# Kernel optimization log

Measured on AMD Instinct MI355X. Metric: run time of the kernel, lower is better.

Reference implementation:

```python
import jax, jax.numpy as jnp
import numpy as np

K = 1.0          # manifold curvature parameter (Lorentz hyperboloid <x,x>_L = -K)
NUM_HEADS = 16
LN_EPS = 1e-5
MID_EPS = 1e-8


def add_time(space):
    # lift a space-like vector onto the hyperboloid: x0 = sqrt(||s||^2 + K)
    t = jnp.sqrt(jnp.sum(space * space, axis=-1, keepdims=True) + K)
    return jnp.concatenate([t, space], axis=-1)


def hlinear(x, W, b):
    # Lorentz linear: dense map on full ambient vector -> space part, recompute time
    return add_time(jnp.einsum('...d,od->...o', x, W) + b)


def hyp_layernorm(x, g, b):
    s = x[..., 1:]
    mu = jnp.mean(s, axis=-1, keepdims=True)
    var = jnp.mean((s - mu) ** 2, axis=-1, keepdims=True)
    s = (s - mu) * jax.lax.rsqrt(var + LN_EPS) * g + b
    return add_time(s)


def hyp_relu(x):
    return add_time(jax.nn.relu(x[..., 1:]))


def lorentz_norm(v):
    # sqrt(|<v,v>_L|) with clamp for numerical safety
    inner = -v[..., 0] ** 2 + jnp.sum(v[..., 1:] ** 2, axis=-1)
    return jnp.sqrt(jnp.maximum(jnp.abs(inner), MID_EPS))


def midpoint_pair(z, x):
    # manifold.midpoint(stack([z, x], dim=-2)).squeeze(): mean then project back
    ave = 0.5 * (z + x)
    return jnp.sqrt(K) * ave / lorentz_norm(ave)[..., None]


def attention(x, Wq, bq, Wk, bk, Wv, bv, Wo, bo):
    B, S, D = x.shape
    dim = D - 1
    H = NUM_HEADS
    dh = dim // H

    def split_heads(t):
        # drop time, split space into heads, re-lift each head onto hyperboloid
        s = t[..., 1:].reshape(B, S, H, dh).transpose(0, 2, 1, 3)  # [B,H,S,dh]
        return add_time(s)                                          # [B,H,S,dh+1]

    qh = split_heads(hlinear(x, Wq, bq))
    kh = split_heads(hlinear(x, Wk, bk))
    vh = split_heads(hlinear(x, Wv, bv))

    # pairwise Lorentz inner product; scores = -d_L^2 / sqrt(dh)
    inner = (jnp.einsum('bhid,bhjd->bhij', qh[..., 1:], kh[..., 1:])
             - qh[..., 0][..., :, None] * kh[..., 0][..., None, :])
    scores = (2.0 / K + 2.0 * inner) / jnp.sqrt(jnp.asarray(dh, x.dtype))
    att = jax.nn.softmax(scores, axis=-1)

    # Lorentz midpoint aggregation of values (weights sum to 1)
    ave = jnp.einsum('bhij,bhjd->bhid', att, vh)
    out = jnp.sqrt(K) * ave / lorentz_norm(ave)[..., None]  # [B,H,S,dh+1]

    # concat head space parts, re-lift, output projection
    out_space = out[..., 1:].transpose(0, 2, 1, 3).reshape(B, S, dim)
    return hlinear(add_time(out_space), Wo, bo)


def reference(x, Wq, bq, Wk, bk, Wv, bv, Wo, bo, ln1_g, ln1_b, W1, c1, W2, c2, ln2_g, ln2_b):
    z = attention(x, Wq, bq, Wk, bk, Wv, bv, Wo, bo)
    x = midpoint_pair(z, x)
    x = hyp_layernorm(x, ln1_g, ln1_b)
    h = hyp_relu(hlinear(x, W1, c1))
    z = hlinear(h, W2, c2)
    x = midpoint_pair(z, x)
    x = hyp_layernorm(x, ln2_g, ln2_b)
    return x


def setup_inputs() -> dict:
    key = jax.random.key(0)
    ks = jax.random.split(key, 12)
    B, S, dim, mlp = 4, 1024, 1024, 4096
    D = dim + 1
    sc = 0.02
    x = add_time(jax.random.normal(ks[0], (B, S, dim), dtype=jnp.float32))
    return {
        'x': x,
        'Wq': sc * jax.random.normal(ks[1], (dim, D), dtype=jnp.float32),
        'bq': jnp.zeros((dim,), jnp.float32),
        'Wk': sc * jax.random.normal(ks[2], (dim, D), dtype=jnp.float32),
        'bk': jnp.zeros((dim,), jnp.float32),
        'Wv': sc * jax.random.normal(ks[3], (dim, D), dtype=jnp.float32),
        'bv': jnp.zeros((dim,), jnp.float32),
        'Wo': sc * jax.random.normal(ks[4], (dim, D), dtype=jnp.float32),
        'bo': jnp.zeros((dim,), jnp.float32),
        'ln1_g': jnp.ones((dim,), jnp.float32),
        'ln1_b': jnp.zeros((dim,), jnp.float32),
        'W1': sc * jax.random.normal(ks[5], (mlp, D), dtype=jnp.float32),
        'c1': jnp.zeros((mlp,), jnp.float32),
        'W2': sc * jax.random.normal(ks[6], (dim, mlp + 1), dtype=jnp.float32),
        'c2': jnp.zeros((dim,), jnp.float32),
        'ln2_g': jnp.ones((dim,), jnp.float32),
        'ln2_b': jnp.zeros((dim,), jnp.float32),
    }
```

## Files before the change

### kernel.cpp

```cpp
#include <hip/hip_runtime.h>

typedef unsigned short u16;
typedef unsigned int   u32;
typedef short bf16x8 __attribute__((ext_vector_type(8)));
typedef float f32x4  __attribute__((ext_vector_type(4)));

#define NTOK 4096
#define SEQ  1024

__device__ __forceinline__ u16 f2bf(float f){
  union { float f; u32 u; } x; x.f = f;
  u32 r = (x.u + 0x7FFFu + ((x.u >> 16) & 1u)) >> 16;
  return (u16)r;
}
__device__ __forceinline__ float bf2f(u16 u){
  union { u32 u; float f; } x; x.u = ((u32)u) << 16; return x.f;
}
__device__ __forceinline__ void gl_lds16(const void* gp, void* lp){
  __builtin_amdgcn_global_load_lds(
      (const __attribute__((address_space(1))) u32*)gp,
      (__attribute__((address_space(3))) u32*)lp, 16, 0, 0);
}

__global__ __launch_bounds__(256) void conv_x(const float* __restrict__ x,
                                              u16* __restrict__ xs, float* __restrict__ xt){
  int t = blockIdx.x * 256 + threadIdx.x;
  int tok = t >> 10, i = t & 1023;
  xs[t] = f2bf(x[(size_t)tok * 1025 + 1 + i]);
  if (i == 0) xt[tok] = x[(size_t)tok * 1025];
}

__global__ __launch_bounds__(256) void conv_w_all(
    const float* __restrict__ Wq, const float* __restrict__ Wk,
    const float* __restrict__ Wv, const float* __restrict__ Wo,
    const float* __restrict__ W1, const float* __restrict__ W2,
    u16* __restrict__ wqkv, u16* __restrict__ wo_s, u16* __restrict__ w1_s, u16* __restrict__ w2_s,
    float* __restrict__ wqkv0, float* __restrict__ wo0, float* __restrict__ w10, float* __restrict__ w20)
{
  int t = blockIdx.x * 256 + threadIdx.x;
  const int M1 = 1 << 20;
  const float* W; u16* Wb; float* w0; int shift; int idx;
  if (t < 4 * M1){
    int region = t >> 20; idx = t & (M1 - 1); shift = 10;
    if (region == 0)      { W = Wq; Wb = wqkv;          w0 = wqkv0; }
    else if (region == 1) { W = Wk; Wb = wqkv + M1;     w0 = wqkv0 + 1024; }
    else if (region == 2) { W = Wv; Wb = wqkv + 2 * M1; w0 = wqkv0 + 2048; }
    else                  { W = Wo; Wb = wo_s;          w0 = wo0; }
  } else if (t < 8 * M1){
    idx = t - 4 * M1; shift = 10; W = W1; Wb = w1_s; w0 = w10;
  } else {
    idx = t - 8 * M1; shift = 12; W = W2; Wb = w2_s; w0 = w20;
  }
  int Kin = 1 << shift;
  int r = idx >> shift, i = idx & (Kin - 1);
  Wb[idx] = f2bf(W[(size_t)r * (Kin + 1) + 1 + i]);
  if (i == 0) w0[r] = W[(size_t)r * (Kin + 1)];
}

__global__ __launch_bounds__(256) void v_transpose(const u16* __restrict__ qkv,
                                                   const float* __restrict__ vtm,
                                                   u16* __restrict__ vT){
  __shared__ u16 tile[64 * 72];
  const int tid = threadIdx.x;
  const int kt = blockIdx.x, bh = blockIdx.y;
  const int b = bh >> 4, h = bh & 15;
  #pragma unroll
  for (int i = 0; i < 2; i++){
    int c = tid * 2 + i;
    int key = c >> 3, fc = c & 7;
    uint4 v = *(const uint4*)(qkv + ((size_t)(b * 1024 + kt * 64 + key)) * 3072 + 2048 + h * 64 + fc * 8);
    *(uint4*)&tile[key * 72 + fc * 8] = v;
  }
  __syncthreads();
  for (int c = tid; c < 520; c += 256){
    int vtr = c >> 3, kc = c & 7;
    union { uint4 v; u16 s[8]; } d;
    if (vtr == 0){
      #pragma unroll
      for (int j = 0; j < 8; j++) d.s[j] = f2bf(vtm[(size_t)bh * 1024 + kt * 64 + kc * 8 + j]);
    } else {
      int f = vtr - 1;
      #pragma unroll
      for (int j = 0; j < 8; j++) d.s[j] = tile[(kc * 8 + j) * 72 + f];
    }
    *(uint4*)(vT + ((size_t)bh * 65 + vtr) * 1024 + kt * 64 + kc * 8) = d.v;
  }
}

__global__ __launch_bounds__(256) void gemm_bt(
    const u16* __restrict__ A, int lda, const u16* __restrict__ Bm, int ldb,
    const float* __restrict__ at, int at_mode, const float* __restrict__ b0,
    const float* __restrict__ bias_a, const float* __restrict__ bias_b, const float* __restrict__ bias_c,
    u16* __restrict__ Cbf, int ldc, int Kslice, int mode,
    float* __restrict__ qtv, float* __restrict__ ktv, float* __restrict__ vtm,
    float* __restrict__ rowsq)
{
  __shared__ u16 As[2][128 * 32];
  __shared__ u16 Bs[2][128 * 32];
  const int tid = threadIdx.x;
  const int w = tid >> 6, l = tid & 63;
  const int l15 = l & 15, q = l >> 4;
  const int m0 = blockIdx.y * 128, n0 = blockIdx.x * 128;
  const int ks = blockIdx.z;
  const int kbeg = ks * Kslice;
  const int kend = kbeg + Kslice;
  const int wr = w >> 1, wc = w & 1;
  f32x4 acc[4][4] = {};

  auto stage = [&](int kt, int buf){
    #pragma unroll
    for (int i = 0; i < 2; i++){
      int s = (w * 2 + i) * 64 + l;
      int row = s >> 2;
      int kc = ((s & 3) - (s >> 3)) & 3;
      gl_lds16(A  + (size_t)(m0 + row) * lda + kt + kc * 8, &As[buf][(w * 2 + i) * 512]);
      gl_lds16(Bm + (size_t)(n0 + row) * ldb + kt + kc * 8, &Bs[buf][(w * 2 + i) * 512]);
    }
  };
  auto compute = [&](int buf){
    bf16x8 af[4], bfr[4];
    #pragma unroll
    for (int i = 0; i < 4; i++){
      int row = wr * 64 + i * 16 + l15;
      int slot = row * 4 + ((q + (row >> 1)) & 3);
      af[i] = *(const bf16x8*)&As[buf][slot * 8];
    }
    #pragma unroll
    for (int j = 0; j < 4; j++){
      int row = wc * 64 + j * 16 + l15;
      int slot = row * 4 + ((q + (row >> 1)) & 3);
      bfr[j] = *(const bf16x8*)&Bs[buf][slot * 8];
    }
    #pragma unroll
    for (int i = 0; i < 4; i++)
      #pragma unroll
      for (int j = 0; j < 4; j++)
        acc[i][j] = __builtin_amdgcn_mfma_f32_16x16x32_bf16(af[i], bfr[j], acc[i][j], 0, 0, 0);
  };

  stage(kbeg, 0);
  for (int kt = kbeg; kt < kend; kt += 64){
    __syncthreads();
    if (kt + 32 < kend) stage(kt + 32, 1);
    compute(0);
    __syncthreads();
    if (kt + 64 < kend) stage(kt + 64, 0);
    compute(1);
  }

  const size_t slice_off = (size_t)ks * (size_t)(gridDim.y * 128) * ldc;
  #pragma unroll
  for (int i = 0; i < 4; i++){
    float atv[4];
    #pragma unroll
    for (int r = 0; r < 4; r++){
      float a = at[m0 + wr * 64 + i * 16 + q * 4 + r];
      atv[r] = at_mode ? sqrtf(a + 1.f) : a;
    }
    float p[4] = {0.f, 0.f, 0.f, 0.f};
    #pragma unroll
    for (int j = 0; j < 4; j++){
      int col = n0 + wc * 64 + j * 16 + l15;
      float b0v = b0[col];
      float bv;
      if (mode == 0) bv = (col < 1024) ? bias_a[col] : (col < 2048) ? bias_b[col - 1024] : bias_c[col - 2048];
      else bv = bias_a[col];
      #pragma unroll
      for (int r = 0; r < 4; r++){
        size_t row = (size_t)(m0 + wr * 64 + i * 16 + q * 4 + r);
        float add = (ks == 0) ? (atv[r] * b0v + bv) : 0.f;
        float v = acc[i][j][r] + add;
        if (mode == 2) v = fmaxf(v, 0.f);
        Cbf[slice_off + row * ldc + col] = f2bf(v);
        if (mode != 1) p[r] += v * v;
      }
    }
    if (mode != 1){
      #pragma unroll
      for (int r = 0; r < 4; r++){
        float s = p[r];
        s += __shfl_xor(s, 1, 64); s += __shfl_xor(s, 2, 64);
        s += __shfl_xor(s, 4, 64); s += __shfl_xor(s, 8, 64);
        if (l15 == 0){
          int row = m0 + wr * 64 + i * 16 + q * 4 + r;
          if (mode == 2){
            atomicAdd(&rowsq[row], s);
          } else {
            int ch = (n0 + wc * 64) >> 6;
            int bb = row >> 10, sidx = row & 1023;
            float t = sqrtf(s + 1.f);
            if (ch < 16)      qtv[((size_t)bb * 16 + ch) * 1024 + sidx] = t;
            else if (ch < 32) ktv[((size_t)bb * 16 + ch - 16) * 1024 + sidx] = t;
            else              vtm[((size_t)bb * 16 + ch - 32) * 1024 + sidx] = t;
          }
        }
      }
    }
  }
}

__global__ __launch_bounds__(512) void attn_kernel(
    const u16* __restrict__ qkv, const float* __restrict__ qt,
    const float* __restrict__ ktm, const u16* __restrict__ vT,
    u16* __restrict__ aout, float* __restrict__ aot_sq)
{
  __shared__ u16 Qlds[8192];
  __shared__ u16 Klds[4096];
  __shared__ u16 Vlds[5120];
  __shared__ u16 Plds[9216];
  const int tid = threadIdx.x;
  const int w = tid >> 6, l = tid & 63;
  const int l15 = l & 15, qd = l >> 4;
  const int q0 = blockIdx.x * 128;
  const int bh = blockIdx.y;
  const int b = bh >> 4, h = bh & 15;
  const size_t tokbase = (size_t)b << 10;

  #pragma unroll
  for (int i = 0; i < 2; i++){
    int c = i * 512 + w * 64 + l;
    int row = c >> 3, kc = ((c & 7) - row) & 7;
    gl_lds16(qkv + (tokbase + q0 + row) * 3072 + h * 64 + kc * 8, &Qlds[(i * 512 + w * 64) * 8]);
  }
  __syncthreads();
  bf16x8 aq[2];
  {
    int row = w * 16 + l15;
    #pragma unroll
    for (int kk = 0; kk < 2; kk++)
      aq[kk] = *(const bf16x8*)&Qlds[(row * 8 + ((kk * 4 + qd + row) & 7)) * 8];
  }
  float tq[4];
  #pragma unroll
  for (int r = 0; r < 4; r++)
    tq[r] = qt[(size_t)bh * SEQ + q0 + w * 16 + qd * 4 + r];

  float mrow[4] = {-1e30f, -1e30f, -1e30f, -1e30f};
  f32x4 acco[5] = {};

  for (int kt = 0; kt < 16; kt++){
    __syncthreads();
    {
      int c = w * 64 + l;
      int row = c >> 3, kc = ((c & 7) - row) & 7;
      gl_lds16(qkv + (tokbase + kt * 64 + row) * 3072 + 1024 + h * 64 + kc * 8, &Klds[w * 512]);
      gl_lds16(vT + ((size_t)bh * 65 + row) * 1024 + kt * 64 + kc * 8, &Vlds[w * 512]);
    }
    if (w == 0 && l < 8){
      gl_lds16(vT + ((size_t)bh * 65 + 64) * 1024 + kt * 64 + (l & 7) * 8, &Vlds[4096]);
    }
    __syncthreads();

    float sc[4][4];
    float mx[4] = {-1e30f, -1e30f, -1e30f, -1e30f};
    #pragma unroll
    for (int ct = 0; ct < 4; ct++){
      f32x4 z = {0.f, 0.f, 0.f, 0.f};
      int key = ct * 16 + l15;
      #pragma unroll
      for (int kk = 0; kk < 2; kk++){
        bf16x8 bk = *(const bf16x8*)&Klds[(key * 8 + ((kk * 4 + qd + key) & 7)) * 8];
        z = __builtin_amdgcn_mfma_f32_16x16x32_bf16(aq[kk], bk, z, 0, 0, 0);
      }
      float tk = ktm[(size_t)bh * SEQ + kt * 64 + key];
      #pragma unroll
      for (int r = 0; r < 4; r++){
        float s = 0.25f + 0.25f * (z[r] - tq[r] * tk);
        sc[ct][r] = s;
        mx[r] = fmaxf(mx[r], s);
      }
    }
    #pragma unroll
    for (int r = 0; r < 4; r++){
      #pragma unroll
      for (int msk = 1; msk < 16; msk <<= 1)
        mx[r] = fmaxf(mx[r], __shfl_xor(mx[r], msk, 64));
      float mnew = fmaxf(mrow[r], mx[r]);
      float alpha = __expf(mrow[r] - mnew);
      mrow[r] = mnew;
      #pragma unroll
      for (int co = 0; co < 5; co++) acco[co][r] *= alpha;
      mx[r] = mnew;
    }
    #pragma unroll
    for (int ct = 0; ct < 4; ct++)
      #pragma unroll
      for (int r = 0; r < 4; r++)
        Plds[w * 1152 + (qd * 4 + r) * 72 + ct * 16 + l15] = f2bf(__expf(sc[ct][r] - mx[r]));
    asm volatile("s_waitcnt lgkmcnt(0)" ::: "memory");
    bf16x8 ap[2];
    #pragma unroll
    for (int kk = 0; kk < 2; kk++)
      ap[kk] = *(const bf16x8*)&Plds[w * 1152 + l15 * 72 + kk * 32 + qd * 8];
    #pragma unroll
    for (int co = 0; co < 5; co++){
      int vtr = co * 16 + l15;
      #pragma unroll
      for (int kk = 0; kk < 2; kk++){
        bf16x8 bv = *(const bf16x8*)&Vlds[(vtr * 8 + ((kk * 4 + qd + vtr) & 7)) * 8];
        acco[co] = __builtin_amdgcn_mfma_f32_16x16x32_bf16(ap[kk], bv, acco[co], 0, 0, 0);
      }
    }
  }
  #pragma unroll
  for (int r = 0; r < 4; r++){
    float ss = 0.f;
    #pragma unroll
    for (int co = 0; co < 5; co++){
      int col = co * 16 + l15;
      float v = acco[co][r];
      if (col == 0) ss -= v * v;
      else if (col < 65) ss += v * v;
    }
    #pragma unroll
    for (int msk = 1; msk < 16; msk <<= 1) ss += __shfl_xor(ss, msk, 64);
    float v0b = __shfl(acco[0][r], l & 48, 64);
    float sp = ss + v0b * v0b;
    float rn = rsqrtf(fmaxf(fabsf(ss), 1e-8f));
    size_t rowg = tokbase + q0 + w * 16 + qd * 4 + r;
    if (l15 == 0) atomicAdd(&aot_sq[rowg], sp * rn * rn);
    #pragma unroll
    for (int co = 0; co < 5; co++){
      int col = co * 16 + l15;
      if (col >= 1 && col < 65)
        aout[rowg * 1024 + h * 64 + col - 1] = f2bf(acco[co][r] * rn);
    }
  }
}

__device__ __forceinline__ float block_sum(float v, float* red){
  int tid = threadIdx.x;
  #pragma unroll
  for (int m = 1; m < 64; m <<= 1) v += __shfl_xor(v, m, 64);
  __syncthreads();
  if ((tid & 63) == 0) red[tid >> 6] = v;
  __syncthreads();
  return red[0] + red[1] + red[2] + red[3];
}

__global__ __launch_bounds__(256) void mid_ln(
    const u16* __restrict__ z, const float* __restrict__ xfull,
    const u16* __restrict__ xsb, const float* __restrict__ xtv,
    const float* __restrict__ gam, const float* __restrict__ bet,
    u16* __restrict__ ob, float* __restrict__ ot,
    float* __restrict__ ofull, int mode_x, int mode_out, int nsl)
{
  __shared__ float red[4];
  const int tid = threadIdx.x;
  const int tok = blockIdx.x;
  float zv[4], xv[4], xtime;
  if (mode_x == 0){
    const float* xr = xfull + (size_t)tok * 1025;
    xtime = xr[0];
    #pragma unroll
    for (int j = 0; j < 4; j++) xv[j] = xr[1 + tid + j * 256];
  } else {
    xtime = xtv[tok];
    const u16* xr = xsb + (size_t)tok * 1024;
    #pragma unroll
    for (int j = 0; j < 4; j++) xv[j] = bf2f(xr[tid + j * 256]);
  }
  {
    #pragma unroll
    for (int j = 0; j < 4; j++) zv[j] = 0.f;
    for (int s = 0; s < nsl; s++){
      const u16* zs = z + (size_t)s * NTOK * 1024 + (size_t)tok * 1024;
      #pragma unroll
      for (int j = 0; j < 4; j++) zv[j] += bf2f(zs[tid + j * 256]);
    }
  }
  float ssz = 0.f;
  #pragma unroll
  for (int j = 0; j < 4; j++) ssz += zv[j] * zv[j];
  ssz = block_sum(ssz, red);
  float tz = sqrtf(ssz + 1.f);
  float av[4]; float ssa = 0.f;
  #pragma unroll
  for (int j = 0; j < 4; j++){ av[j] = 0.5f * (zv[j] + xv[j]); ssa += av[j] * av[j]; }
  ssa = block_sum(ssa, red);
  float avt = 0.5f * (tz + xtime);
  float rn = rsqrtf(fmaxf(fabsf(ssa - avt * avt), 1e-8f));
  float uv[4]; float su = 0.f, squ = 0.f;
  #pragma unroll
  for (int j = 0; j < 4; j++){ uv[j] = av[j] * rn; su += uv[j]; squ += uv[j] * uv[j]; }
  su = block_sum(su, red);
  squ = block_sum(squ, red);
  float mu = su * (1.f / 1024.f);
  float var = squ * (1.f / 1024.f) - mu * mu;
  float rv = rsqrtf(fmaxf(var, 0.f) + 1e-5f);
  float sv[4]; float sss = 0.f;
  #pragma unroll
  for (int j = 0; j < 4; j++){
    int i = tid + j * 256;
    sv[j] = (uv[j] - mu) * rv * gam[i] + bet[i];
    sss += sv[j] * sv[j];
  }
  sss = block_sum(sss, red);
  float tout = sqrtf(sss + 1.f);
  if (mode_out == 0){
    #pragma unroll
    for (int j = 0; j < 4; j++){
      int i = tid + j * 256;
      ob[(size_t)tok * 1024 + i] = f2bf(sv[j]);
    }
    if (tid == 0) ot[tok] = tout;
  } else {
    float* orow = ofull + (size_t)tok * 1025;
    #pragma unroll
    for (int j = 0; j < 4; j++) orow[1 + tid + j * 256] = sv[j];
    if (tid == 0) orow[0] = tout;
  }
}

extern "C" void kernel_launch(void* const* d_in, const int* in_sizes, int n_in,
                              void* d_out, int out_size, void* d_ws, size_t ws_size,
                              hipStream_t stream){
  const float* x   = (const float*)d_in[0];
  const float* Wq  = (const float*)d_in[1];
  const float* bq  = (const float*)d_in[2];
  const float* Wk  = (const float*)d_in[3];
  const float* bk  = (const float*)d_in[4];
  const float* Wv  = (const float*)d_in[5];
  const float* bv  = (const float*)d_in[6];
  const float* Wo  = (const float*)d_in[7];
  const float* bo  = (const float*)d_in[8];
  const float* g1  = (const float*)d_in[9];
  const float* be1 = (const float*)d_in[10];
  const float* W1  = (const float*)d_in[11];
  const float* c1  = (const float*)d_in[12];
  const float* W2  = (const float*)d_in[13];
  const float* c2  = (const float*)d_in[14];
  const float* g2  = (const float*)d_in[15];
  const float* be2 = (const float*)d_in[16];
  float* out = (float*)d_out;

  char* p = (char*)d_ws;
  auto take = [&](size_t n){ char* r = p; p += (n + 255) & ~(size_t)255; return r; };
  u16*   xs    = (u16*)  take((size_t)NTOK * 1024 * 2);
  float* xt    = (float*)take(NTOK * 4);
  u16*   wqkv  = (u16*)  take((size_t)3072 * 1024 * 2);
  float* wqkv0 = (float*)take(3072 * 4);
  u16*   wo_s  = (u16*)  take((size_t)1024 * 1024 * 2);
  float* wo0   = (float*)take(1024 * 4);
  u16*   w1_s  = (u16*)  take((size_t)4096 * 1024 * 2);
  float* w10   = (float*)take(4096 * 4);
  u16*   w2_s  = (u16*)  take((size_t)1024 * 4096 * 2);
  float* w20   = (float*)take(1024 * 4);
  u16*   qkvb  = (u16*)  take((size_t)NTOK * 3072 * 2);
  float* qtv   = (float*)take((size_t)64 * 1024 * 4);
  float* ktv   = (float*)take((size_t)64 * 1024 * 4);
  float* vtm   = (float*)take((size_t)64 * 1024 * 4);
  u16*   vT    = (u16*)  take((size_t)64 * 65 * 1024 * 2);
  u16*   aoutb = (u16*)  take((size_t)NTOK * 1024 * 2);
  float* sqbuf = (float*)take((size_t)2 * NTOK * 4);
  float* aot_sq = sqbuf;
  float* htv_sq = sqbuf + NTOK;
  u16*   zbuf  = (u16*)  take((size_t)4 * NTOK * 1024 * 2);
  u16*   x1b   = (u16*)  take((size_t)NTOK * 1024 * 2);
  float* x1t   = (float*)take(NTOK * 4);
  u16*   hbuf  = (u16*)  take((size_t)NTOK * 4096 * 2);

  hipMemsetAsync(sqbuf, 0, (size_t)2 * NTOK * 4, stream);

  conv_x<<<NTOK * 1024 / 256, 256, 0, stream>>>(x, xs, xt);
  conv_w_all<<<(12 * 1024 * 1024) / 256, 256, 0, stream>>>(
      Wq, Wk, Wv, Wo, W1, W2, wqkv, wo_s, w1_s, w2_s, wqkv0, wo0, w10, w20);

  gemm_bt<<<dim3(24, 32), 256, 0, stream>>>(xs, 1024, wqkv, 1024, xt, 0, wqkv0,
      bq, bk, bv, qkvb, 3072, 1024, 0, qtv, ktv, vtm, nullptr);
  v_transpose<<<dim3(16, 64), 256, 0, stream>>>(qkvb, vtm, vT);
  attn_kernel<<<dim3(8, 64), 512, 0, stream>>>(qkvb, qtv, ktv, vT, aoutb, aot_sq);
  gemm_bt<<<dim3(8, 32, 2), 256, 0, stream>>>(aoutb, 1024, wo_s, 1024, aot_sq, 1, wo0,
      bo, nullptr, nullptr, zbuf, 1024, 512, 1, nullptr, nullptr, nullptr, nullptr);
  mid_ln<<<NTOK, 256, 0, stream>>>(zbuf, x, nullptr, nullptr, g1, be1,
      x1b, x1t, nullptr, 0, 0, 2);
  gemm_bt<<<dim3(32, 32), 256, 0, stream>>>(x1b, 1024, w1_s, 1024, x1t, 0, w10,
      c1, nullptr, nullptr, hbuf, 4096, 1024, 2, nullptr, nullptr, nullptr, htv_sq);
  gemm_bt<<<dim3(8, 32, 4), 256, 0, stream>>>(hbuf, 4096, w2_s, 4096, htv_sq, 1, w20,
      c2, nullptr, nullptr, zbuf, 1024, 1024, 1, nullptr, nullptr, nullptr, nullptr);
  mid_ln<<<NTOK, 256, 0, stream>>>(zbuf, nullptr, x1b, x1t, g2, be2,
      nullptr, nullptr, out, 1, 1, 4);
}
```

Measured before the change: 448.3 us.

## Double-buffer attention K/V loads, deepen GEMM k-stage, read bf16 residual in first LN

The GEMM now stages 64-wide k chunks per buffer (two 32-wide halves), halving the barrier count per k iteration while doubling LDS use. The attention kernel double-buffers K and V tiles in a shared LDS arena, prefetching the next tile before computing the current one and dropping one barrier per iteration; the second V buffer aliases the Q region after Q has been loaded into registers. The first mid_ln reads the residual from the bf16 copy of x instead of the fp32 input, which cuts memory traffic but lowers residual precision.

```diff
diff --git a/kernel.cpp b/kernel.cpp
--- a/kernel.cpp
+++ b/kernel.cpp
@@ -95,8 +95,8 @@
     float* __restrict__ qtv, float* __restrict__ ktv, float* __restrict__ vtm,
     float* __restrict__ rowsq)
 {
-  __shared__ u16 As[2][128 * 32];
-  __shared__ u16 Bs[2][128 * 32];
+  __shared__ u16 As[2][128 * 64];
+  __shared__ u16 Bs[2][128 * 64];
   const int tid = threadIdx.x;
   const int w = tid >> 6, l = tid & 63;
   const int l15 = l & 15, q = l >> 4;
@@ -109,27 +109,32 @@
 
   auto stage = [&](int kt, int buf){
     #pragma unroll
-    for (int i = 0; i < 2; i++){
-      int s = (w * 2 + i) * 64 + l;
-      int row = s >> 2;
-      int kc = ((s & 3) - (s >> 3)) & 3;
-      gl_lds16(A  + (size_t)(m0 + row) * lda + kt + kc * 8, &As[buf][(w * 2 + i) * 512]);
-      gl_lds16(Bm + (size_t)(n0 + row) * ldb + kt + kc * 8, &Bs[buf][(w * 2 + i) * 512]);
+    for (int half = 0; half < 2; half++){
+      #pragma unroll
+      for (int i = 0; i < 2; i++){
+        int s = (w * 2 + i) * 64 + l;
+        int row = s >> 2;
+        int kc = ((s & 3) - (s >> 3)) & 3;
+        gl_lds16(A  + (size_t)(m0 + row) * lda + kt + half * 32 + kc * 8,
+                 &As[buf][half * 4096 + (w * 2 + i) * 512]);
+        gl_lds16(Bm + (size_t)(n0 + row) * ldb + kt + half * 32 + kc * 8,
+                 &Bs[buf][half * 4096 + (w * 2 + i) * 512]);
+      }
     }
   };
-  auto compute = [&](int buf){
+  auto compute = [&](int buf, int half){
     bf16x8 af[4], bfr[4];
     #pragma unroll
     for (int i = 0; i < 4; i++){
       int row = wr * 64 + i * 16 + l15;
       int slot = row * 4 + ((q + (row >> 1)) & 3);
-      af[i] = *(const bf16x8*)&As[buf][slot * 8];
+      af[i] = *(const bf16x8*)&As[buf][half * 4096 + slot * 8];
     }
     #pragma unroll
     for (int j = 0; j < 4; j++){
       int row = wc * 64 + j * 16 + l15;
       int slot = row * 4 + ((q + (row >> 1)) & 3);
-      bfr[j] = *(const bf16x8*)&Bs[buf][slot * 8];
+      bfr[j] = *(const bf16x8*)&Bs[buf][half * 4096 + slot * 8];
     }
     #pragma unroll
     for (int i = 0; i < 4; i++)
@@ -139,13 +144,13 @@
   };
 
   stage(kbeg, 0);
-  for (int kt = kbeg; kt < kend; kt += 64){
+  for (int kt = kbeg; kt < kend; kt += 128){
     __syncthreads();
-    if (kt + 32 < kend) stage(kt + 32, 1);
-    compute(0);
+    if (kt + 64 < kend) stage(kt + 64, 1);
+    compute(0, 0); compute(0, 1);
     __syncthreads();
-    if (kt + 64 < kend) stage(kt + 64, 0);
-    compute(1);
+    if (kt + 128 < kend) stage(kt + 128, 0);
+    compute(1, 0); compute(1, 1);
   }
 
   const size_t slice_off = (size_t)ks * (size_t)(gridDim.y * 128) * ldc;
@@ -204,10 +209,13 @@
     const float* __restrict__ ktm, const u16* __restrict__ vT,
     u16* __restrict__ aout, float* __restrict__ aot_sq)
 {
-  __shared__ u16 Qlds[8192];
-  __shared__ u16 Klds[4096];
-  __shared__ u16 Vlds[5120];
-  __shared__ u16 Plds[9216];
+  __shared__ u16 smem[30720];
+  u16* Qlds = smem;
+  u16* Kl0 = smem + 8192;
+  u16* Kl1 = smem + 12288;
+  u16* Vl0 = smem + 16384;
+  u16* Vl1 = smem;
+  u16* Plds = smem + 21504;
   const int tid = threadIdx.x;
   const int w = tid >> 6, l = tid & 63;
   const int l15 = l & 15, qd = l >> 4;
@@ -235,21 +243,26 @@
   for (int r = 0; r < 4; r++)
     tq[r] = qt[(size_t)bh * SEQ + q0 + w * 16 + qd * 4 + r];
 
+  auto stage_kv = [&](int kt, int buf){
+    u16* K = buf ? Kl1 : Kl0;
+    u16* V = buf ? Vl1 : Vl0;
+    int c = w * 64 + l;
+    int row = c >> 3, kc = ((c & 7) - row) & 7;
+    gl_lds16(qkv + (tokbase + kt * 64 + row) * 3072 + 1024 + h * 64 + kc * 8, &K[w * 512]);
+    gl_lds16(vT + ((size_t)bh * 65 + row) * 1024 + kt * 64 + kc * 8, &V[w * 512]);
+    if (w == 0 && l < 8)
+      gl_lds16(vT + ((size_t)bh * 65 + 64) * 1024 + kt * 64 + (l & 7) * 8, &V[4096]);
+  };
+
   float mrow[4] = {-1e30f, -1e30f, -1e30f, -1e30f};
   f32x4 acco[5] = {};
 
+  stage_kv(0, 0);
   for (int kt = 0; kt < 16; kt++){
     __syncthreads();
-    {
-      int c = w * 64 + l;
-      int row = c >> 3, kc = ((c & 7) - row) & 7;
-      gl_lds16(qkv + (tokbase + kt * 64 + row) * 3072 + 1024 + h * 64 + kc * 8, &Klds[w * 512]);
-      gl_lds16(vT + ((size_t)bh * 65 + row) * 1024 + kt * 64 + kc * 8, &Vlds[w * 512]);
-    }
-    if (w == 0 && l < 8){
-      gl_lds16(vT + ((size_t)bh * 65 + 64) * 1024 + kt * 64 + (l & 7) * 8, &Vlds[4096]);
-    }
-    __syncthreads();
+    if (kt + 1 < 16) stage_kv(kt + 1, (kt + 1) & 1);
+    u16* K = (kt & 1) ? Kl1 : Kl0;
+    u16* V = (kt & 1) ? Vl1 : Vl0;
 
     float sc[4][4];
     float mx[4] = {-1e30f, -1e30f, -1e30f, -1e30f};
@@ -259,7 +272,7 @@
       int key = ct * 16 + l15;
       #pragma unroll
       for (int kk = 0; kk < 2; kk++){
-        bf16x8 bk = *(const bf16x8*)&Klds[(key * 8 + ((kk * 4 + qd + key) & 7)) * 8];
+        bf16x8 bk = *(const bf16x8*)&K[(key * 8 + ((kk * 4 + qd + key) & 7)) * 8];
         z = __builtin_amdgcn_mfma_f32_16x16x32_bf16(aq[kk], bk, z, 0, 0, 0);
       }
       float tk = ktm[(size_t)bh * SEQ + kt * 64 + key];
@@ -297,7 +310,7 @@
       int vtr = co * 16 + l15;
       #pragma unroll
       for (int kk = 0; kk < 2; kk++){
-        bf16x8 bv = *(const bf16x8*)&Vlds[(vtr * 8 + ((kk * 4 + qd + vtr) & 7)) * 8];
+        bf16x8 bv = *(const bf16x8*)&V[(vtr * 8 + ((kk * 4 + qd + vtr) & 7)) * 8];
         acco[co] = __builtin_amdgcn_mfma_f32_16x16x32_bf16(ap[kk], bv, acco[co], 0, 0, 0);
       }
     }
@@ -339,23 +352,17 @@
 }
 
 __global__ __launch_bounds__(256) void mid_ln(
-    const u16* __restrict__ z, const float* __restrict__ xfull,
-    const u16* __restrict__ xsb, const float* __restrict__ xtv,
+    const u16* __restrict__ z, const u16* __restrict__ xsb, const float* __restrict__ xtv,
     const float* __restrict__ gam, const float* __restrict__ bet,
     u16* __restrict__ ob, float* __restrict__ ot,
-    float* __restrict__ ofull, int mode_x, int mode_out, int nsl)
+    float* __restrict__ ofull, int mode_out, int nsl)
 {
   __shared__ float red[4];
   const int tid = threadIdx.x;
   const int tok = blockIdx.x;
   float zv[4], xv[4], xtime;
-  if (mode_x == 0){
-    const float* xr = xfull + (size_t)tok * 1025;
-    xtime = xr[0];
-    #pragma unroll
-    for (int j = 0; j < 4; j++) xv[j] = xr[1 + tid + j * 256];
-  } else {
-    xtime = xtv[tok];
+  xtime = xtv[tok];
+  {
     const u16* xr = xsb + (size_t)tok * 1024;
     #pragma unroll
     for (int j = 0; j < 4; j++) xv[j] = bf2f(xr[tid + j * 256]);
@@ -472,12 +479,12 @@
   attn_kernel<<<dim3(8, 64), 512, 0, stream>>>(qkvb, qtv, ktv, vT, aoutb, aot_sq);
   gemm_bt<<<dim3(8, 32, 2), 256, 0, stream>>>(aoutb, 1024, wo_s, 1024, aot_sq, 1, wo0,
       bo, nullptr, nullptr, zbuf, 1024, 512, 1, nullptr, nullptr, nullptr, nullptr);
-  mid_ln<<<NTOK, 256, 0, stream>>>(zbuf, x, nullptr, nullptr, g1, be1,
-      x1b, x1t, nullptr, 0, 0, 2);
+  mid_ln<<<NTOK, 256, 0, stream>>>(zbuf, xs, xt, g1, be1,
+      x1b, x1t, nullptr, 0, 2);
   gemm_bt<<<dim3(32, 32), 256, 0, stream>>>(x1b, 1024, w1_s, 1024, x1t, 0, w10,
       c1, nullptr, nullptr, hbuf, 4096, 1024, 2, nullptr, nullptr, nullptr, htv_sq);
   gemm_bt<<<dim3(8, 32, 4), 256, 0, stream>>>(hbuf, 4096, w2_s, 4096, htv_sq, 1, w20,
       c2, nullptr, nullptr, zbuf, 1024, 1024, 1, nullptr, nullptr, nullptr, nullptr);
-  mid_ln<<<NTOK, 256, 0, stream>>>(zbuf, nullptr, x1b, x1t, g2, be2,
-      nullptr, nullptr, out, 1, 1, 4);
-}
+  mid_ln<<<NTOK, 256, 0, stream>>>(zbuf, x1b, x1t, g2, be2,
+      nullptr, nullptr, out, 1, 4);
+}
```

Measured after the change: 431.2 us. -3.8%, faster.
